# Optimization experiments

Measured on AMD Instinct MI355X. Metric: run time of the kernel, lower is better.

The kernel has to match this reference:

```python
import jax, jax.numpy as jnp
import numpy as np

B, C_IM, N_IN, H, W = 4, 3, 2, 256, 256
NC, MR, NH, NB = 25, 2, 64, 10  # n_class, m_range, num_hidden, num blocks


def _conv(x, w, pad, dil=1):
    return jax.lax.conv_general_dilated(
        x, w, (1, 1), [(pad, pad), (pad, pad)], rhs_dilation=(dil, dil),
        dimension_numbers=('NCHW', 'OIHW', 'NCHW'))


def _bn(x, g, b, m, v):
    # inference-mode BatchNorm2d, eps=1e-5
    inv = g / jnp.sqrt(v + 1e-5)
    return x * inv[:, None, None] + (b - m * inv)[:, None, None]


def setup_inputs() -> dict:
    key = jax.random.key(0)
    ks = iter(jax.random.split(key, 40))
    rn = lambda s, sc=0.05: jax.random.normal(next(ks), s, jnp.float32) * sc
    ru = lambda s: jax.random.uniform(next(ks), s, jnp.float32)
    return {
        'im_input_f': rn((B, C_IM * N_IN, H, W), 1.0),
        'im_input_b': rn((B, C_IM * N_IN, H, W), 1.0),
        'ones': jnp.ones((B, 1, H, W), jnp.float32),
        'm_kernel': ru((1, NC, 2 * MR + 1, 2 * MR + 1)),
        'bn0_g': ru((C_IM * N_IN,)), 'bn0_b': rn((C_IM * N_IN,)),
        'bn0_m': rn((C_IM * N_IN,)), 'bn0_v': ru((C_IM * N_IN,)),
        'conv0_w': rn((NH, C_IM * N_IN, 3, 3)),
        'blk_bn1_g': ru((NB, NH)), 'blk_bn1_b': rn((NB, NH)),
        'blk_bn1_m': rn((NB, NH)), 'blk_bn1_v': ru((NB, NH)),
        'blk_w11': rn((NB, NH, NH, 3, 3)), 'blk_w12': rn((NB, NH, NH, 3, 3)),
        'blk_bn2_g': ru((NB, NH)), 'blk_bn2_b': rn((NB, NH)),
        'blk_bn2_m': rn((NB, NH)), 'blk_bn2_v': ru((NB, NH)),
        'blk_w2': rn((NB, NH, NH, 3, 3)),
        'bnf_g': ru((NH,)), 'bnf_b': rn((NH,)),
        'bnf_m': rn((NH,)), 'bnf_v': ru((NH,)),
        'convf_w': rn((NC, NH, 3, 3)), 'convf_b': rn((NC,)),
    }


def reference(im_input_f, im_input_b, ones, m_kernel,
              bn0_g, bn0_b, bn0_m, bn0_v, conv0_w,
              blk_bn1_g, blk_bn1_b, blk_bn1_m, blk_bn1_v, blk_w11, blk_w12,
              blk_bn2_g, blk_bn2_b, blk_bn2_m, blk_bn2_v, blk_w2,
              bnf_g, bnf_b, bnf_m, bnf_v, convf_w, convf_b):

    def backbone(x):
        x = _conv(_bn(x, bn0_g, bn0_b, bn0_m, bn0_v), conv0_w, 1)

        def block(h, p):
            g1, b1, m1, v1, w11, w12, g2, b2, m2, v2, w2 = p
            out = jax.nn.relu(_bn(h, g1, b1, m1, v1))
            out = _conv(out, w11, 1) + _conv(out, w12, 2, 2)
            out = _conv(jax.nn.relu(_bn(out, g2, b2, m2, v2)), w2, 1)
            return h + out, None

        x, _ = jax.lax.scan(block, x, (blk_bn1_g, blk_bn1_b, blk_bn1_m,
                                       blk_bn1_v, blk_w11, blk_w12,
                                       blk_bn2_g, blk_bn2_b, blk_bn2_m,
                                       blk_bn2_v, blk_w2))
        return _conv(jax.nn.relu(_bn(x, bnf_g, bnf_b, bnf_m, bnf_v)),
                     convf_w, 1) + convf_b[:, None, None]

    motion_f = backbone(im_input_f)
    motion_b = backbone(im_input_b)
    mask_f = jax.nn.softmax(motion_f, axis=1)  # [B, NC, H, W]
    mask_b = jax.nn.softmax(motion_b, axis=1)

    def seg(mask):  # construct_seg, fully batched
        return _conv(ones * mask, m_kernel, MR)  # [B, 1, H, W]

    def pred_im(im_last, mask):  # construct_image: fold (B, im_channel) into batch
        x = (im_last[:, :, None] * mask[:, None]).reshape(B * C_IM, NC, H, W)
        return _conv(x, m_kernel, MR).reshape(B, C_IM, H, W)

    seg_f = seg(mask_f)
    seg_b = seg(mask_b)
    pred_f = pred_im(im_input_f[:, -C_IM:], mask_f)
    pred_b = pred_im(im_input_b[:, -C_IM:], mask_b)
    attn = (seg_f + 1e-5) / (seg_f + seg_b + 2e-5)
    pred = attn * pred_f + (1 - attn) * pred_b
    return (pred, pred_f, mask_f, attn, pred_b, mask_b, 1 - attn)
```

## Files before the change

kernel.cpp:

```cpp
#include <hip/hip_runtime.h>
#include <stdint.h>

typedef unsigned short u16;
typedef float f4 __attribute__((ext_vector_type(4)));
typedef float f16v __attribute__((ext_vector_type(16)));
typedef short s8v __attribute__((ext_vector_type(8)));

static __device__ __forceinline__ float bf2f(u16 u){ return __uint_as_float(((unsigned)u)<<16); }
static __device__ __forceinline__ u16 f2bf(float f){
  unsigned u = __float_as_uint(f);
  unsigned r = u + 0x7fffu + ((u>>16)&1u);
  return (u16)(r>>16);
}

#define WS_H    0ull
#define WS_T    67108864ull
#define WS_WDH  134217728ull
#define WS_WDL  135692288ull
#define WS_W2H  137166848ull
#define WS_W2L  137904128ull
#define WS_W0T  138641408ull
#define WS_WFT  138655232ull
#define WS_PAR  138728960ull

#define S0 0
#define T0 8
#define S1 16
#define T1 656
#define S2 1296
#define T2 1936
#define SF 2576
#define TF 2640
#define MK 2704
#define CB 3332

#define O_PRED   0ull
#define O_PREDF  786432ull
#define O_MASKF  1572864ull
#define O_ATTN   8126464ull
#define O_PREDB  8388608ull
#define O_MASKB  9175040ull
#define O_OMA    15728640ull

__global__ void k_prep(const float* g0,const float* b0,const float* m0,const float* v0,
                       const float* g1,const float* b1,const float* m1,const float* v1,
                       const float* g2,const float* b2,const float* m2,const float* v2,
                       const float* gf,const float* bf_,const float* mf,const float* vf,
                       const float* mk,const float* cb, float* par){
  for (int i = threadIdx.x; i < 640; i += 256){
    if (i < 6){ float s = g0[i]/sqrtf(v0[i]+1e-5f); par[S0+i]=s; par[T0+i]=b0[i]-m0[i]*s; }
    { float s = g1[i]/sqrtf(v1[i]+1e-5f); par[S1+i]=s; par[T1+i]=b1[i]-m1[i]*s; }
    { float s = g2[i]/sqrtf(v2[i]+1e-5f); par[S2+i]=s; par[T2+i]=b2[i]-m2[i]*s; }
    if (i < 64){ float s = gf[i]/sqrtf(vf[i]+1e-5f); par[SF+i]=s; par[TF+i]=bf_[i]-mf[i]*s; }
    if (i < 625) par[MK+i] = mk[i];
    if (i < 25)  par[CB+i] = cb[i];
  }
}

__global__ void k_wx2(const float* wf,const float* w0, float* wft, float* w0t){
  int e = blockIdx.x*256 + threadIdx.x;
  if (e < 3456){
    int o = e & 63, r = e >> 6;
    int tap = r % 9, c = r / 9;
    w0t[e] = w0[(o*6+c)*9 + tap];
  } else if (e < 3456 + 18432){
    int e4 = e - 3456;
    int o = e4 & 31, r = e4 >> 5;
    int tap = r % 9, c = r / 9;
    wft[e4] = (o < 25) ? wf[(o*64+c)*9 + tap] : 0.f;
  }
}

__global__ void k_wxm(const float* w11, const float* w12, const float* w2,
                      u16* wdH, u16* wdL, u16* w2H, u16* w2L){
  int e = blockIdx.x*256 + threadIdx.x;
  if (e < 737280){
    int j = e & 7, l = (e>>3) & 63, cog = (e>>9) & 1, kc = (e>>10) & 1;
    int idx2 = e >> 11;
    int tf = idx2 % 36, b = idx2 / 36;
    int tap = tf % 18, h = tf / 18;
    int co = cog*32 + (l & 31);
    int ci = h*32 + kc*16 + (l>>5)*8 + j;
    float w = (tap < 9) ? w11[((b*64+co)*64+ci)*9 + tap]
                        : w12[((b*64+co)*64+ci)*9 + (tap-9)];
    u16 hi = f2bf(w);
    wdH[e] = hi; wdL[e] = f2bf(w - bf2f(hi));
  } else if (e < 1105920){
    int e2 = e - 737280;
    int j = e2 & 7, l = (e2>>3) & 63, cog = (e2>>9) & 1, kc = (e2>>10) & 1;
    int idx2 = e2 >> 11;
    int tf = idx2 % 18, b = idx2 / 18;
    int tap = tf % 9, h = tf / 9;
    int co = cog*32 + (l & 31);
    int ci = h*32 + kc*16 + (l>>5)*8 + j;
    float w = w2[((b*64+co)*64+ci)*9 + tap];
    u16 hi = f2bf(w);
    w2H[e2] = hi; w2L[e2] = f2bf(w - bf2f(hi));
  }
}

template<int NT,int TAPSET,int OUTMODE>
__global__ __launch_bounds__(256,2) void k_mconv(
    const float* __restrict__ in, float* __restrict__ outb,
    const u16* __restrict__ wH, const u16* __restrict__ wL,
    const float* __restrict__ sc_, const float* __restrict__ tc_){
  __shared__ __align__(16) u16 ldsH[432*32];
  __shared__ __align__(16) u16 ldsL[432*32];
  __shared__ float lsc[64], ltc[64];
  const int t = threadIdx.x;
  if (t < 64){ lsc[t] = sc_[t]; ltc[t] = tc_[t]; }
  __syncthreads();
  const int img = blockIdx.z, ox = blockIdx.x*32, oy = blockIdx.y*8;
  const int lane = t & 63, wv = t >> 6;
  const int xcol = lane & 31, g = lane >> 5;
  f16v acc[2][2];
  #pragma unroll
  for (int r=0;r<2;r++)
    #pragma unroll
    for (int cg=0;cg<2;cg++) acc[r][cg] = (f16v)(0.f);
  const s8v* wH8 = (const s8v*)wH;
  const s8v* wL8 = (const s8v*)wL;

  #pragma unroll 1
  for (int h = 0; h < 2; ++h){
    if (h) __syncthreads();
    for (int idx = t; idx < 1728; idx += 256){
      int oct = idx / 432, px = idx % 432;
      int pr = px / 36, pc = px % 36;
      int gy = oy + pr - 2, gx = ox + pc - 2;
      int cb = h*32 + oct*8;
      s8v vh = {0,0,0,0,0,0,0,0}, vl = {0,0,0,0,0,0,0,0};
      if ((unsigned)gy < 256u && (unsigned)gx < 256u){
        const float* ip = in + (((size_t)(img*64 + cb))<<16) + gy*256 + gx;
        #pragma unroll
        for (int k=0;k<8;k++){
          float v = fmaxf(ip[(size_t)k<<16]*lsc[cb+k] + ltc[cb+k], 0.f);
          u16 hi = f2bf(v);
          vh[k] = (short)hi;
          vl[k] = (short)f2bf(v - bf2f(hi));
        }
      }
      int ad = (px*64 + oct*16) ^ ((px&7)<<4);
      *(s8v*)((char*)ldsH + ad) = vh;
      *(s8v*)((char*)ldsL + ad) = vl;
    }
    __syncthreads();
    #pragma unroll
    for (int tap = 0; tap < NT; ++tap){
      int dy, dx;
      if (TAPSET==0){
        if (tap < 9){ dy = tap/3 - 1; dx = tap%3 - 1; }
        else { int dd = tap-9; dy = 2*(dd/3 - 1); dx = 2*(dd%3 - 1); }
      } else { dy = tap/3 - 1; dx = tap%3 - 1; }
      const int tf = h*NT + tap;
      #pragma unroll
      for (int kc = 0; kc < 2; ++kc){
        s8v ah0 = wH8[(size_t)(((tf*2 + kc)*2 + 0)*64 + lane)];
        s8v ah1 = wH8[(size_t)(((tf*2 + kc)*2 + 1)*64 + lane)];
        s8v al0 = wL8[(size_t)(((tf*2 + kc)*2 + 0)*64 + lane)];
        s8v al1 = wL8[(size_t)(((tf*2 + kc)*2 + 1)*64 + lane)];
        #pragma unroll
        for (int r = 0; r < 2; ++r){
          int px = (wv*2 + r + dy + 2)*36 + (xcol + dx + 2);
          int ad = (px*64 + kc*32 + g*16) ^ ((px&7)<<4);
          s8v xh = *(const s8v*)((const char*)ldsH + ad);
          s8v xl = *(const s8v*)((const char*)ldsL + ad);
          acc[r][0] = __builtin_amdgcn_mfma_f32_32x32x16_bf16(ah0, xh, acc[r][0], 0,0,0);
          acc[r][1] = __builtin_amdgcn_mfma_f32_32x32x16_bf16(ah1, xh, acc[r][1], 0,0,0);
          acc[r][0] = __builtin_amdgcn_mfma_f32_32x32x16_bf16(al0, xh, acc[r][0], 0,0,0);
          acc[r][1] = __builtin_amdgcn_mfma_f32_32x32x16_bf16(al1, xh, acc[r][1], 0,0,0);
          acc[r][0] = __builtin_amdgcn_mfma_f32_32x32x16_bf16(ah0, xl, acc[r][0], 0,0,0);
          acc[r][1] = __builtin_amdgcn_mfma_f32_32x32x16_bf16(ah1, xl, acc[r][1], 0,0,0);
        }
      }
    }
  }

  #pragma unroll
  for (int r=0;r<2;r++){
    int y = oy + wv*2 + r;
    int x = ox + xcol;
    #pragma unroll
    for (int cg=0;cg<2;cg++){
      #pragma unroll
      for (int j=0;j<16;j++){
        int co = cg*32 + (j&3) + 8*(j>>2) + 4*g;
        size_t o = (((size_t)(img*64 + co))<<16) + (size_t)(y*256 + x);
        if (OUTMODE==0) outb[o] = acc[r][cg][j];
        else            outb[o] += acc[r][cg][j];
      }
    }
  }
}

template<int NTAPS,int TAPSET,int OUTMODE,int RELU>
__global__ __launch_bounds__(256) void k_conv(
    const float* __restrict__ in, float* __restrict__ outb,
    const float* __restrict__ wt, const float* __restrict__ sc_,
    const float* __restrict__ tc_, int nci){
  __shared__ float lin[4*12*20];
  __shared__ float lw[4*NTAPS*64];
  __shared__ float lsc[64], ltc[64];
  const int t = threadIdx.x;
  const int img = blockIdx.z;
  const int ox = blockIdx.x*16, oy = blockIdx.y*8;
  if (t < 64 && t < nci){ lsc[t] = sc_[t]; ltc[t] = tc_[t]; }
  const int wv = t>>6, lane = t&63;
  const int row = lane>>4, col = lane&15;
  const int co0 = wv*16;
  const int pb0 = (row+2)*20 + col + 2;
  const int pb1 = pb0 + 80;
  f4 a0[4], a1[4];
  #pragma unroll
  for (int q=0;q<4;q++){ a0[q] = f4{0.f,0.f,0.f,0.f}; a1[q] = f4{0.f,0.f,0.f,0.f}; }

  #pragma unroll 1
  for (int c0=0; c0<nci; c0+=4){
    const int cc = (nci - c0 < 4) ? (nci - c0) : 4;
    __syncthreads();
    for (int idx=t; idx<cc*240; idx+=256){
      int c = idx/240, rr = (idx/20)%12, xx = idx%20;
      int gy = oy + rr - 2, gx = ox + xx - 2;
      float v = 0.f;
      if ((unsigned)gy < 256u && (unsigned)gx < 256u){
        v = in[(size_t)(img*nci + c0 + c)*65536 + gy*256 + gx]*lsc[c0+c] + ltc[c0+c];
        if (RELU) v = fmaxf(v, 0.f);
      }
      lin[idx] = v;
    }
    {
      const f4* ws4 = (const f4*)(wt + (size_t)c0*NTAPS*64);
      f4* lw4 = (f4*)lw;
      for (int idx=t; idx<cc*NTAPS*16; idx+=256) lw4[idx] = ws4[idx];
    }
    __syncthreads();
    #pragma unroll 1
    for (int c=0; c<cc; c++){
      const float* lpc = lin + c*240;
      const float* lwc = lw + c*NTAPS*64 + co0;
      #pragma unroll
      for (int tap=0; tap<NTAPS; tap++){
        int dy, dx;
        if (TAPSET==0){
          if (tap < 9){ dy = tap/3 - 1; dx = tap%3 - 1; }
          else      { dy = 2*((tap-9)/3-1); dx = 2*((tap-9)%3-1); }
        } else { dy = tap/3 - 1; dx = tap%3 - 1; }
        float v0 = lpc[pb0 + dy*20 + dx];
        float v1 = lpc[pb1 + dy*20 + dx];
        const f4* wp = (const f4*)(lwc + tap*64);
        #pragma unroll
        for (int q=0;q<4;q++){
          f4 w = wp[q];
          a0[q] += v0*w;
          a1[q] += v1*w;
        }
      }
    }
  }

  size_t p0 = (size_t)((oy+row)*256 + ox + col);
  size_t base = (size_t)(img*64 + co0)*65536;
  if (OUTMODE==0){
    #pragma unroll
    for (int q=0;q<4;q++)
      #pragma unroll
      for (int j=0;j<4;j++){
        outb[base + (size_t)(q*4+j)*65536 + p0]        = a0[q][j];
        outb[base + (size_t)(q*4+j)*65536 + p0 + 1024] = a1[q][j];
      }
  } else {
    #pragma unroll
    for (int q=0;q<4;q++)
      #pragma unroll
      for (int j=0;j<4;j++){
        size_t o0 = base + (size_t)(q*4+j)*65536 + p0;
        outb[o0]        += a0[q][j];
        outb[o0 + 1024] += a1[q][j];
      }
  }
}

__global__ __launch_bounds__(256) void k_fin2(const float* __restrict__ in,
    const float* __restrict__ wft, const float* __restrict__ par,
    float* __restrict__ dmask){
  __shared__ float lin[4*20*20];
  __shared__ float lw[4*9*32];
  __shared__ float lsc[64], ltc[64];
  const int t = threadIdx.x;
  const int img = blockIdx.z;
  const int ox = blockIdx.x*16, oy = blockIdx.y*16;
  if (t < 64){ lsc[t] = par[SF+t]; ltc[t] = par[TF+t]; }
  const int row = t>>4, col = t&15;
  const int pb = (row+2)*20 + col + 2;
  f4 a[8];
  #pragma unroll
  for (int q=0;q<8;q++) a[q] = f4{0.f,0.f,0.f,0.f};

  #pragma unroll 1
  for (int c0=0; c0<64; c0+=4){
    __syncthreads();
    for (int idx=t; idx<4*400; idx+=256){
      int c = idx/400, rr = (idx/20)%20, xx = idx%20;
      int gy = oy + rr - 2, gx = ox + xx - 2;
      float v = 0.f;
      if ((unsigned)gy < 256u && (unsigned)gx < 256u)
        v = fmaxf(in[(size_t)(img*64 + c0 + c)*65536 + gy*256 + gx]*lsc[c0+c] + ltc[c0+c], 0.f);
      lin[idx] = v;
    }
    {
      const f4* ws4 = (const f4*)(wft + (size_t)c0*288);
      f4* lw4 = (f4*)lw;
      for (int idx=t; idx<288; idx+=256) lw4[idx] = ws4[idx];
    }
    __syncthreads();
    #pragma unroll 1
    for (int c=0; c<4; c++){
      const float* lpc = lin + c*400;
      const float* lwc = lw + c*288;
      #pragma unroll
      for (int tap=0; tap<9; tap++){
        int dy = tap/3 - 1, dx = tap%3 - 1;
        float v = lpc[pb + dy*20 + dx];
        const f4* wp = (const f4*)(lwc + tap*32);
        #pragma unroll
        for (int q=0;q<8;q++) a[q] += v*wp[q];
      }
    }
  }

  float lg[25];
  float mx = -3.4e38f;
  #pragma unroll
  for (int o=0;o<25;o++){ lg[o] = a[o>>2][o&3] + par[CB+o]; mx = fmaxf(mx, lg[o]); }
  float s = 0.f;
  #pragma unroll
  for (int o=0;o<25;o++){ lg[o] = expf(lg[o]-mx); s += lg[o]; }
  float inv = 1.f/s;
  size_t p0 = (size_t)((oy+row)*256 + ox + col);
  #pragma unroll
  for (int o=0;o<25;o++)
    dmask[(size_t)(img*25+o)*65536 + p0] = lg[o]*inv;
}

__global__ __launch_bounds__(256) void k_blend(const float* __restrict__ msk,
    const float* __restrict__ imf, const float* __restrict__ imb,
    const float* __restrict__ ones_in, const float* __restrict__ par,
    float* __restrict__ out){
  int bid = blockIdx.x;
  int swz = (bid & 7)*128 + (bid >> 3);
  int img = swz >> 8, y = swz & 255, x = threadIdx.x;
  int p = y*256 + x;
  int aofs[25]; unsigned vm = 0u;
  #pragma unroll
  for (int tap=0; tap<25; tap++){
    int dy = tap/5-2, dx = tap%5-2, yy = y+dy, xx = x+dx;
    bool okb = ((unsigned)yy < 256u) && ((unsigned)xx < 256u);
    aofs[tap] = okb ? (yy*256+xx) : 0;
    vm |= (okb ? 1u : 0u) << tap;
  }
  float sff[25], sfb[25];
  #pragma unroll
  for (int i=0;i<25;i++){ sff[i]=0.f; sfb[i]=0.f; }
  #pragma unroll 1
  for (int k=0;k<25;k++){
    const float* mF = msk + O_MASKF + ((size_t)(img*25+k)<<16);
    const float* mB = msk + O_MASKB + ((size_t)(img*25+k)<<16);
    #pragma unroll
    for (int tap=0; tap<25; tap++){
      float mkv = par[MK + k*25 + tap];
      float vF = (vm >> tap & 1u) ? mF[aofs[tap]] : 0.f;
      float vB = (vm >> tap & 1u) ? mB[aofs[tap]] : 0.f;
      sff[tap] += mkv*vF;
      sfb[tap] += mkv*vB;
    }
  }
  float segf = 0.f, segb = 0.f;
  float pf[3] = {0.f,0.f,0.f}, pb[3] = {0.f,0.f,0.f};
  size_t ib = ((size_t)(img*6))<<16;
  #pragma unroll
  for (int tap=0; tap<25; tap++){
    if (vm >> tap & 1u){
      float one = ones_in[((size_t)img<<16) + (size_t)aofs[tap]];
      segf += one*sff[tap]; segb += one*sfb[tap];
      #pragma unroll
      for (int c=0;c<3;c++){
        pf[c] += imf[ib + ((size_t)(3+c)<<16) + (size_t)aofs[tap]] * sff[tap];
        pb[c] += imb[ib + ((size_t)(3+c)<<16) + (size_t)aofs[tap]] * sfb[tap];
      }
    }
  }
  float attn = (segf + 1e-5f)/(segf + segb + 2e-5f);
  float na = 1.f - attn;
  #pragma unroll
  for (int c=0;c<3;c++){
    size_t off = (size_t)(img*3+c)*65536 + p;
    out[O_PRED  + off] = attn*pf[c] + na*pb[c];
    out[O_PREDF + off] = pf[c];
    out[O_PREDB + off] = pb[c];
  }
  size_t oa = ((size_t)img<<16) + (size_t)p;
  out[O_ATTN + oa] = attn;
  out[O_OMA  + oa] = na;
}

extern "C" void kernel_launch(void* const* d_in, const int* in_sizes, int n_in,
                              void* d_out, int out_size, void* d_ws, size_t ws_size,
                              hipStream_t stream){
  (void)in_sizes; (void)n_in; (void)out_size; (void)ws_size;
  char* ws = (char*)d_ws;
  float* h   = (float*)(ws + WS_H);
  float* tb  = (float*)(ws + WS_T);
  u16*  wdH  = (u16*)(ws + WS_WDH);
  u16*  wdL  = (u16*)(ws + WS_WDL);
  u16*  w2H  = (u16*)(ws + WS_W2H);
  u16*  w2L  = (u16*)(ws + WS_W2L);
  float* w0t = (float*)(ws + WS_W0T);
  float* wft = (float*)(ws + WS_WFT);
  float* par = (float*)(ws + WS_PAR);
  float* out = (float*)d_out;

  k_prep<<<1,256,0,stream>>>((const float*)d_in[4],(const float*)d_in[5],(const float*)d_in[6],(const float*)d_in[7],
                             (const float*)d_in[9],(const float*)d_in[10],(const float*)d_in[11],(const float*)d_in[12],
                             (const float*)d_in[15],(const float*)d_in[16],(const float*)d_in[17],(const float*)d_in[18],
                             (const float*)d_in[20],(const float*)d_in[21],(const float*)d_in[22],(const float*)d_in[23],
                             (const float*)d_in[3],(const float*)d_in[25], par);
  k_wx2<<<86,256,0,stream>>>((const float*)d_in[24],(const float*)d_in[8], wft, w0t);
  k_wxm<<<4320,256,0,stream>>>((const float*)d_in[13],(const float*)d_in[14],(const float*)d_in[19],
                               wdH, wdL, w2H, w2L);

  dim3 g0(16,32,4);
  dim3 gm(8,32,4);
  dim3 gf(16,16,4);
  for (int dir=0; dir<2; dir++){
    const float* im = (const float*)d_in[dir];
    float* dmask = out + (dir ? O_MASKB : O_MASKF);
    k_conv<9,1,0,0><<<g0,256,0,stream>>>(im, h, w0t, par+S0, par+T0, 6);
    for (int b=0;b<10;b++){
      k_mconv<18,0,0><<<gm,256,0,stream>>>(h, tb, wdH + (size_t)b*73728, wdL + (size_t)b*73728,
                                           par + S1 + b*64, par + T1 + b*64);
      k_mconv<9,1,1><<<gm,256,0,stream>>>(tb, h, w2H + (size_t)b*36864, w2L + (size_t)b*36864,
                                          par + S2 + b*64, par + T2 + b*64);
    }
    k_fin2<<<gf,256,0,stream>>>(h, wft, par, dmask);
  }
  k_blend<<<1024,256,0,stream>>>(out, (const float*)d_in[0], (const float*)d_in[1],
                                 (const float*)d_in[2], par, out);
}
```

Before: 4.417 ms.

## Repartition MFMA conv waves by output-channel group and move final conv to MFMA

The block-conv kernel now assigns each wave one 32-channel output group over four rows instead of both groups over two rows, which halves the weight fragments each wave loads and adds software prefetch of the next tap's weights. The final 64->25 conv with softmax, previously a scalar FP32 kernel, now runs on the same split-bf16 MFMA path with a fused softmax epilogue that uses lane shuffles. Weight prep for the final conv moves into the bf16 hi/lo split kernel. The trade-off is more LDS activation reads per wave, and the final conv pads 25 output channels to 32.

```diff
diff --git a/kernel.cpp b/kernel.cpp
--- a/kernel.cpp
+++ b/kernel.cpp
@@ -20,7 +20,8 @@
 #define WS_W2H  137166848ull
 #define WS_W2L  137904128ull
 #define WS_W0T  138641408ull
-#define WS_WFT  138655232ull
+#define WS_WFH  138655232ull
+#define WS_WFL  138692096ull
 #define WS_PAR  138728960ull
 
 #define S0 0
@@ -57,22 +58,17 @@
   }
 }
 
-__global__ void k_wx2(const float* wf,const float* w0, float* wft, float* w0t){
+__global__ void k_wx2(const float* w0, float* w0t){
   int e = blockIdx.x*256 + threadIdx.x;
   if (e < 3456){
     int o = e & 63, r = e >> 6;
     int tap = r % 9, c = r / 9;
     w0t[e] = w0[(o*6+c)*9 + tap];
-  } else if (e < 3456 + 18432){
-    int e4 = e - 3456;
-    int o = e4 & 31, r = e4 >> 5;
-    int tap = r % 9, c = r / 9;
-    wft[e4] = (o < 25) ? wf[(o*64+c)*9 + tap] : 0.f;
-  }
-}
-
-__global__ void k_wxm(const float* w11, const float* w12, const float* w2,
-                      u16* wdH, u16* wdL, u16* w2H, u16* w2L){
+  }
+}
+
+__global__ void k_wxm(const float* w11, const float* w12, const float* w2, const float* wf,
+                      u16* wdH, u16* wdL, u16* w2H, u16* w2L, u16* wfH, u16* wfL){
   int e = blockIdx.x*256 + threadIdx.x;
   if (e < 737280){
     int j = e & 7, l = (e>>3) & 63, cog = (e>>9) & 1, kc = (e>>10) & 1;
@@ -96,34 +92,44 @@
     float w = w2[((b*64+co)*64+ci)*9 + tap];
     u16 hi = f2bf(w);
     w2H[e2] = hi; w2L[e2] = f2bf(w - bf2f(hi));
-  }
-}
-
-template<int NT,int TAPSET,int OUTMODE>
-__global__ __launch_bounds__(256,2) void k_mconv(
+  } else if (e < 1124352){
+    int e3 = e - 1105920;
+    int j = e3 & 7, l = (e3>>3) & 63, kc = (e3>>9) & 1, tf = e3 >> 10;
+    int tap = tf % 9, h = tf / 9;
+    int co = l & 31;
+    int ci = h*32 + kc*16 + (l>>5)*8 + j;
+    float w = (co < 25) ? wf[(co*64+ci)*9 + tap] : 0.f;
+    u16 hi = f2bf(w);
+    wfH[e3] = hi; wfL[e3] = f2bf(w - bf2f(hi));
+  }
+}
+
+template<int NT,int TAPSET,int OUTMODE,int NCOG>
+__global__ __launch_bounds__(256,2) void k_mc(
     const float* __restrict__ in, float* __restrict__ outb,
     const u16* __restrict__ wH, const u16* __restrict__ wL,
-    const float* __restrict__ sc_, const float* __restrict__ tc_){
+    const float* __restrict__ sc_, const float* __restrict__ tc_,
+    const float* __restrict__ cbv, float* __restrict__ dmask){
+  constexpr int RPW = 2*NCOG;
   __shared__ __align__(16) u16 ldsH[432*32];
   __shared__ __align__(16) u16 ldsL[432*32];
   __shared__ float lsc[64], ltc[64];
   const int t = threadIdx.x;
   if (t < 64){ lsc[t] = sc_[t]; ltc[t] = tc_[t]; }
-  __syncthreads();
   const int img = blockIdx.z, ox = blockIdx.x*32, oy = blockIdx.y*8;
   const int lane = t & 63, wv = t >> 6;
+  const int cog = (NCOG==2) ? (wv & 1) : 0;
+  const int rh  = (NCOG==2) ? (wv >> 1) : wv;
   const int xcol = lane & 31, g = lane >> 5;
-  f16v acc[2][2];
-  #pragma unroll
-  for (int r=0;r<2;r++)
-    #pragma unroll
-    for (int cg=0;cg<2;cg++) acc[r][cg] = (f16v)(0.f);
+  f16v acc[RPW];
+  #pragma unroll
+  for (int r=0;r<RPW;r++) acc[r] = (f16v)(0.f);
   const s8v* wH8 = (const s8v*)wH;
   const s8v* wL8 = (const s8v*)wL;
 
   #pragma unroll 1
   for (int h = 0; h < 2; ++h){
-    if (h) __syncthreads();
+    __syncthreads();
     for (int idx = t; idx < 1728; idx += 256){
       int oct = idx / 432, px = idx % 432;
       int pr = px / 36, pc = px % 36;
@@ -145,66 +151,99 @@
       *(s8v*)((char*)ldsL + ad) = vl;
     }
     __syncthreads();
+
+    s8v ah0, al0, ah1, al1;
+    {
+      size_t o = (size_t)((h*NT*2)*NCOG + cog)*64 + lane;
+      ah0 = wH8[o]; al0 = wL8[o];
+    }
     #pragma unroll
-    for (int tap = 0; tap < NT; ++tap){
+    for (int m = 0; m < 2*NT; ++m){
+      const int tap = m >> 1, kc = m & 1;
       int dy, dx;
       if (TAPSET==0){
         if (tap < 9){ dy = tap/3 - 1; dx = tap%3 - 1; }
         else { int dd = tap-9; dy = 2*(dd/3 - 1); dx = 2*(dd%3 - 1); }
       } else { dy = tap/3 - 1; dx = tap%3 - 1; }
-      const int tf = h*NT + tap;
-      #pragma unroll
-      for (int kc = 0; kc < 2; ++kc){
-        s8v ah0 = wH8[(size_t)(((tf*2 + kc)*2 + 0)*64 + lane)];
-        s8v ah1 = wH8[(size_t)(((tf*2 + kc)*2 + 1)*64 + lane)];
-        s8v al0 = wL8[(size_t)(((tf*2 + kc)*2 + 0)*64 + lane)];
-        s8v al1 = wL8[(size_t)(((tf*2 + kc)*2 + 1)*64 + lane)];
-        #pragma unroll
-        for (int r = 0; r < 2; ++r){
-          int px = (wv*2 + r + dy + 2)*36 + (xcol + dx + 2);
-          int ad = (px*64 + kc*32 + g*16) ^ ((px&7)<<4);
-          s8v xh = *(const s8v*)((const char*)ldsH + ad);
-          s8v xl = *(const s8v*)((const char*)ldsL + ad);
-          acc[r][0] = __builtin_amdgcn_mfma_f32_32x32x16_bf16(ah0, xh, acc[r][0], 0,0,0);
-          acc[r][1] = __builtin_amdgcn_mfma_f32_32x32x16_bf16(ah1, xh, acc[r][1], 0,0,0);
-          acc[r][0] = __builtin_amdgcn_mfma_f32_32x32x16_bf16(al0, xh, acc[r][0], 0,0,0);
-          acc[r][1] = __builtin_amdgcn_mfma_f32_32x32x16_bf16(al1, xh, acc[r][1], 0,0,0);
-          acc[r][0] = __builtin_amdgcn_mfma_f32_32x32x16_bf16(ah0, xl, acc[r][0], 0,0,0);
-          acc[r][1] = __builtin_amdgcn_mfma_f32_32x32x16_bf16(ah1, xl, acc[r][1], 0,0,0);
-        }
-      }
-    }
-  }
-
-  #pragma unroll
-  for (int r=0;r<2;r++){
-    int y = oy + wv*2 + r;
-    int x = ox + xcol;
+      if (m+1 < 2*NT){
+        size_t o = (size_t)(((h*NT + ((m+1)>>1))*2 + ((m+1)&1))*NCOG + cog)*64 + lane;
+        if ((m&1)==0){ ah1 = wH8[o]; al1 = wL8[o]; }
+        else         { ah0 = wH8[o]; al0 = wL8[o]; }
+      }
+      const s8v Ah = ((m&1)==0) ? ah0 : ah1;
+      const s8v Al = ((m&1)==0) ? al0 : al1;
+      #pragma unroll
+      for (int r = 0; r < RPW; ++r){
+        int row = rh*RPW + r;
+        int px = (row + dy + 2)*36 + (xcol + dx + 2);
+        int ad = (px*64 + kc*32 + g*16) ^ ((px&7)<<4);
+        s8v xh = *(const s8v*)((const char*)ldsH + ad);
+        s8v xl = *(const s8v*)((const char*)ldsL + ad);
+        acc[r] = __builtin_amdgcn_mfma_f32_32x32x16_bf16(Ah, xh, acc[r], 0,0,0);
+        acc[r] = __builtin_amdgcn_mfma_f32_32x32x16_bf16(Al, xh, acc[r], 0,0,0);
+        acc[r] = __builtin_amdgcn_mfma_f32_32x32x16_bf16(Ah, xl, acc[r], 0,0,0);
+      }
+    }
+  }
+
+  if (OUTMODE != 2){
     #pragma unroll
-    for (int cg=0;cg<2;cg++){
+    for (int r=0;r<RPW;r++){
+      int y = oy + rh*RPW + r;
+      int x = ox + xcol;
       #pragma unroll
       for (int j=0;j<16;j++){
-        int co = cg*32 + (j&3) + 8*(j>>2) + 4*g;
+        int co = cog*32 + (j&3) + 8*(j>>2) + 4*g;
         size_t o = (((size_t)(img*64 + co))<<16) + (size_t)(y*256 + x);
-        if (OUTMODE==0) outb[o] = acc[r][cg][j];
-        else            outb[o] += acc[r][cg][j];
-      }
-    }
-  }
-}
-
-template<int NTAPS,int TAPSET,int OUTMODE,int RELU>
-__global__ __launch_bounds__(256) void k_conv(
+        if (OUTMODE==0) outb[o] = acc[r][j];
+        else            outb[o] += acc[r][j];
+      }
+    }
+  } else {
+    #pragma unroll
+    for (int r=0;r<RPW;r++){
+      int y = oy + rh*RPW + r;
+      int x = ox + xcol;
+      float lg[16];
+      float mx = -3.4e38f;
+      #pragma unroll
+      for (int j=0;j<16;j++){
+        int co = (j&3) + 8*(j>>2) + 4*g;
+        float v = acc[r][j] + ((co < 25) ? cbv[co] : 0.f);
+        lg[j] = v;
+        if (co < 25) mx = fmaxf(mx, v);
+      }
+      mx = fmaxf(mx, __shfl_xor(mx, 32));
+      float s = 0.f;
+      #pragma unroll
+      for (int j=0;j<16;j++){
+        int co = (j&3) + 8*(j>>2) + 4*g;
+        float e = (co < 25) ? __expf(lg[j]-mx) : 0.f;
+        lg[j] = e; s += e;
+      }
+      s += __shfl_xor(s, 32);
+      float inv = 1.f/s;
+      #pragma unroll
+      for (int j=0;j<16;j++){
+        int co = (j&3) + 8*(j>>2) + 4*g;
+        if (co < 25)
+          dmask[(((size_t)(img*25+co))<<16) + (size_t)(y*256 + x)] = lg[j]*inv;
+      }
+    }
+  }
+}
+
+__global__ __launch_bounds__(256) void k_conv0(
     const float* __restrict__ in, float* __restrict__ outb,
     const float* __restrict__ wt, const float* __restrict__ sc_,
-    const float* __restrict__ tc_, int nci){
+    const float* __restrict__ tc_){
   __shared__ float lin[4*12*20];
-  __shared__ float lw[4*NTAPS*64];
-  __shared__ float lsc[64], ltc[64];
+  __shared__ float lw[4*9*64];
+  __shared__ float lsc[8], ltc[8];
   const int t = threadIdx.x;
   const int img = blockIdx.z;
   const int ox = blockIdx.x*16, oy = blockIdx.y*8;
-  if (t < 64 && t < nci){ lsc[t] = sc_[t]; ltc[t] = tc_[t]; }
+  if (t < 6){ lsc[t] = sc_[t]; ltc[t] = tc_[t]; }
   const int wv = t>>6, lane = t&63;
   const int row = lane>>4, col = lane&15;
   const int co0 = wv*16;
@@ -215,36 +254,30 @@
   for (int q=0;q<4;q++){ a0[q] = f4{0.f,0.f,0.f,0.f}; a1[q] = f4{0.f,0.f,0.f,0.f}; }
 
   #pragma unroll 1
-  for (int c0=0; c0<nci; c0+=4){
-    const int cc = (nci - c0 < 4) ? (nci - c0) : 4;
+  for (int c0=0; c0<6; c0+=4){
+    const int cc = (6 - c0 < 4) ? (6 - c0) : 4;
     __syncthreads();
     for (int idx=t; idx<cc*240; idx+=256){
       int c = idx/240, rr = (idx/20)%12, xx = idx%20;
       int gy = oy + rr - 2, gx = ox + xx - 2;
       float v = 0.f;
-      if ((unsigned)gy < 256u && (unsigned)gx < 256u){
-        v = in[(size_t)(img*nci + c0 + c)*65536 + gy*256 + gx]*lsc[c0+c] + ltc[c0+c];
-        if (RELU) v = fmaxf(v, 0.f);
-      }
+      if ((unsigned)gy < 256u && (unsigned)gx < 256u)
+        v = in[(size_t)(img*6 + c0 + c)*65536 + gy*256 + gx]*lsc[c0+c] + ltc[c0+c];
       lin[idx] = v;
     }
     {
-      const f4* ws4 = (const f4*)(wt + (size_t)c0*NTAPS*64);
+      const f4* ws4 = (const f4*)(wt + (size_t)c0*576);
       f4* lw4 = (f4*)lw;
-      for (int idx=t; idx<cc*NTAPS*16; idx+=256) lw4[idx] = ws4[idx];
+      for (int idx=t; idx<cc*144; idx+=256) lw4[idx] = ws4[idx];
     }
     __syncthreads();
     #pragma unroll 1
     for (int c=0; c<cc; c++){
       const float* lpc = lin + c*240;
-      const float* lwc = lw + c*NTAPS*64 + co0;
-      #pragma unroll
-      for (int tap=0; tap<NTAPS; tap++){
-        int dy, dx;
-        if (TAPSET==0){
-          if (tap < 9){ dy = tap/3 - 1; dx = tap%3 - 1; }
-          else      { dy = 2*((tap-9)/3-1); dx = 2*((tap-9)%3-1); }
-        } else { dy = tap/3 - 1; dx = tap%3 - 1; }
+      const float* lwc = lw + c*576 + co0;
+      #pragma unroll
+      for (int tap=0; tap<9; tap++){
+        int dy = tap/3 - 1, dx = tap%3 - 1;
         float v0 = lpc[pb0 + dy*20 + dx];
         float v1 = lpc[pb1 + dy*20 + dx];
         const f4* wp = (const f4*)(lwc + tap*64);
@@ -260,86 +293,13 @@
 
   size_t p0 = (size_t)((oy+row)*256 + ox + col);
   size_t base = (size_t)(img*64 + co0)*65536;
-  if (OUTMODE==0){
+  #pragma unroll
+  for (int q=0;q<4;q++)
     #pragma unroll
-    for (int q=0;q<4;q++)
-      #pragma unroll
-      for (int j=0;j<4;j++){
-        outb[base + (size_t)(q*4+j)*65536 + p0]        = a0[q][j];
-        outb[base + (size_t)(q*4+j)*65536 + p0 + 1024] = a1[q][j];
-      }
-  } else {
-    #pragma unroll
-    for (int q=0;q<4;q++)
-      #pragma unroll
-      for (int j=0;j<4;j++){
-        size_t o0 = base + (size_t)(q*4+j)*65536 + p0;
-        outb[o0]        += a0[q][j];
-        outb[o0 + 1024] += a1[q][j];
-      }
-  }
-}
-
-__global__ __launch_bounds__(256) void k_fin2(const float* __restrict__ in,
-    const float* __restrict__ wft, const float* __restrict__ par,
-    float* __restrict__ dmask){
-  __shared__ float lin[4*20*20];
-  __shared__ float lw[4*9*32];
-  __shared__ float lsc[64], ltc[64];
-  const int t = threadIdx.x;
-  const int img = blockIdx.z;
-  const int ox = blockIdx.x*16, oy = blockIdx.y*16;
-  if (t < 64){ lsc[t] = par[SF+t]; ltc[t] = par[TF+t]; }
-  const int row = t>>4, col = t&15;
-  const int pb = (row+2)*20 + col + 2;
-  f4 a[8];
-  #pragma unroll
-  for (int q=0;q<8;q++) a[q] = f4{0.f,0.f,0.f,0.f};
-
-  #pragma unroll 1
-  for (int c0=0; c0<64; c0+=4){
-    __syncthreads();
-    for (int idx=t; idx<4*400; idx+=256){
-      int c = idx/400, rr = (idx/20)%20, xx = idx%20;
-      int gy = oy + rr - 2, gx = ox + xx - 2;
-      float v = 0.f;
-      if ((unsigned)gy < 256u && (unsigned)gx < 256u)
-        v = fmaxf(in[(size_t)(img*64 + c0 + c)*65536 + gy*256 + gx]*lsc[c0+c] + ltc[c0+c], 0.f);
-      lin[idx] = v;
-    }
-    {
-      const f4* ws4 = (const f4*)(wft + (size_t)c0*288);
-      f4* lw4 = (f4*)lw;
-      for (int idx=t; idx<288; idx+=256) lw4[idx] = ws4[idx];
-    }
-    __syncthreads();
-    #pragma unroll 1
-    for (int c=0; c<4; c++){
-      const float* lpc = lin + c*400;
-      const float* lwc = lw + c*288;
-      #pragma unroll
-      for (int tap=0; tap<9; tap++){
-        int dy = tap/3 - 1, dx = tap%3 - 1;
-        float v = lpc[pb + dy*20 + dx];
-        const f4* wp = (const f4*)(lwc + tap*32);
-        #pragma unroll
-        for (int q=0;q<8;q++) a[q] += v*wp[q];
-      }
-    }
-  }
-
-  float lg[25];
-  float mx = -3.4e38f;
-  #pragma unroll
-  for (int o=0;o<25;o++){ lg[o] = a[o>>2][o&3] + par[CB+o]; mx = fmaxf(mx, lg[o]); }
-  float s = 0.f;
-  #pragma unroll
-  for (int o=0;o<25;o++){ lg[o] = expf(lg[o]-mx); s += lg[o]; }
-  float inv = 1.f/s;
-  size_t p0 = (size_t)((oy+row)*256 + ox + col);
-  #pragma unroll
-  for (int o=0;o<25;o++)
-    dmask[(size_t)(img*25+o)*65536 + p0] = lg[o]*inv;
+    for (int j=0;j<4;j++){
+      outb[base + (size_t)(q*4+j)*65536 + p0]        = a0[q][j];
+      outb[base + (size_t)(q*4+j)*65536 + p0 + 1024] = a1[q][j];
+    }
 }
 
 __global__ __launch_bounds__(256) void k_blend(const float* __restrict__ msk,
@@ -415,7 +375,8 @@
   u16*  w2H  = (u16*)(ws + WS_W2H);
   u16*  w2L  = (u16*)(ws + WS_W2L);
   float* w0t = (float*)(ws + WS_W0T);
-  float* wft = (float*)(ws + WS_WFT);
+  u16*  wfH  = (u16*)(ws + WS_WFH);
+  u16*  wfL  = (u16*)(ws + WS_WFL);
   float* par = (float*)(ws + WS_PAR);
   float* out = (float*)d_out;
 
@@ -424,24 +385,25 @@
                              (const float*)d_in[15],(const float*)d_in[16],(const float*)d_in[17],(const float*)d_in[18],
                              (const float*)d_in[20],(const float*)d_in[21],(const float*)d_in[22],(const float*)d_in[23],
                              (const float*)d_in[3],(const float*)d_in[25], par);
-  k_wx2<<<86,256,0,stream>>>((const float*)d_in[24],(const float*)d_in[8], wft, w0t);
-  k_wxm<<<4320,256,0,stream>>>((const float*)d_in[13],(const float*)d_in[14],(const float*)d_in[19],
-                               wdH, wdL, w2H, w2L);
+  k_wx2<<<14,256,0,stream>>>((const float*)d_in[8], w0t);
+  k_wxm<<<4392,256,0,stream>>>((const float*)d_in[13],(const float*)d_in[14],(const float*)d_in[19],
+                               (const float*)d_in[24],
+                               wdH, wdL, w2H, w2L, wfH, wfL);
 
   dim3 g0(16,32,4);
   dim3 gm(8,32,4);
-  dim3 gf(16,16,4);
   for (int dir=0; dir<2; dir++){
     const float* im = (const float*)d_in[dir];
     float* dmask = out + (dir ? O_MASKB : O_MASKF);
-    k_conv<9,1,0,0><<<g0,256,0,stream>>>(im, h, w0t, par+S0, par+T0, 6);
+    k_conv0<<<g0,256,0,stream>>>(im, h, w0t, par+S0, par+T0);
     for (int b=0;b<10;b++){
-      k_mconv<18,0,0><<<gm,256,0,stream>>>(h, tb, wdH + (size_t)b*73728, wdL + (size_t)b*73728,
-                                           par + S1 + b*64, par + T1 + b*64);
-      k_mconv<9,1,1><<<gm,256,0,stream>>>(tb, h, w2H + (size_t)b*36864, w2L + (size_t)b*36864,
-                                          par + S2 + b*64, par + T2 + b*64);
-    }
-    k_fin2<<<gf,256,0,stream>>>(h, wft, par, dmask);
+      k_mc<18,0,0,2><<<gm,256,0,stream>>>(h, tb, wdH + (size_t)b*73728, wdL + (size_t)b*73728,
+                                          par + S1 + b*64, par + T1 + b*64, nullptr, nullptr);
+      k_mc<9,1,1,2><<<gm,256,0,stream>>>(tb, h, w2H + (size_t)b*36864, w2L + (size_t)b*36864,
+                                         par + S2 + b*64, par + T2 + b*64, nullptr, nullptr);
+    }
+    k_mc<9,1,2,1><<<gm,256,0,stream>>>(h, nullptr, wfH, wfL,
+                                       par + SF, par + TF, par + CB, dmask);
   }
   k_blend<<<1024,256,0,stream>>>(out, (const float*)d_in[0], (const float*)d_in[1],
                                  (const float*)d_in[2], par, out);
```

Measured after the change: 5.129 ms. +16.1%, slower.
